# Optimization experiments

Measured on AMD Instinct MI355X. Metric: run time of the kernel, lower is better.

## Reference

```python
import jax, jax.numpy as jnp
import numpy as np

H = 1024       # hidden_size
E = 1024       # embedding_size
V = 50257      # output_size (vocab)
L = 64         # max_length


def setup_inputs() -> dict:
    key = jax.random.key(0)
    ks = jax.random.split(key, 12)
    s = 0.02
    return {
        "input": jax.random.randint(ks[0], (1,), 0, V),
        "hidden": jax.random.normal(ks[1], (1, 1, H), dtype=jnp.float32),
        "encoder_outputs": jax.random.normal(ks[2], (L, H), dtype=jnp.float32),
        "emb": jax.random.normal(ks[3], (V, E), dtype=jnp.float32) * s,
        "attn_w": jax.random.normal(ks[4], (L, H + E), dtype=jnp.float32) * s,
        "attn_b": jnp.zeros((L,), dtype=jnp.float32),
        "comb_w": jax.random.normal(ks[5], (E, H + E), dtype=jnp.float32) * s,
        "comb_b": jnp.zeros((E,), dtype=jnp.float32),
        "w_ih": jax.random.normal(ks[6], (3 * H, E), dtype=jnp.float32) * s,
        "b_ih": jnp.zeros((3 * H,), dtype=jnp.float32),
        "w_hh": jax.random.normal(ks[7], (3 * H, H), dtype=jnp.float32) * s,
        "b_hh": jnp.zeros((3 * H,), dtype=jnp.float32),
        "out_w": jax.random.normal(ks[8], (V, H), dtype=jnp.float32) * s,
        "out_b": jnp.zeros((V,), dtype=jnp.float32),
    }


def reference(input, hidden, encoder_outputs, emb, attn_w, attn_b,
              comb_w, comb_b, w_ih, b_ih, w_hh, b_hh, out_w, out_b):
    # embedding + (dropout = identity in eval)
    embedded = emb[input].reshape(1, E)            # [1, E]
    h0 = hidden[0]                                  # [1, H]
    # Bahdanau-style attention over fixed-length encoder outputs
    attn_logits = jnp.concatenate([embedded, h0], axis=1) @ attn_w.T + attn_b
    attn_weights = jax.nn.softmax(attn_logits, axis=1)      # [1, L]
    attn_applied = attn_weights @ encoder_outputs            # [1, H]
    x = jnp.concatenate([embedded, attn_applied], axis=1) @ comb_w.T + comb_b
    x = jax.nn.relu(x)                               # [1, E]
    # single GRU cell step (torch gate order: r, z, n)
    gi = x @ w_ih.T + b_ih
    gh = h0 @ w_hh.T + b_hh
    i_r, i_z, i_n = jnp.split(gi, 3, axis=1)
    h_r, h_z, h_n = jnp.split(gh, 3, axis=1)
    r = jax.nn.sigmoid(i_r + h_r)
    z = jax.nn.sigmoid(i_z + h_z)
    n = jnp.tanh(i_n + r * h_n)
    h_new = (1.0 - z) * n + z * h0                   # [1, H]
    logp = jax.nn.log_softmax(h_new @ out_w.T + out_b, axis=1)  # [1, V]
    return logp, h_new[None], attn_weights
```

## Files before the change

### kernel.cpp

```cpp
#include <hip/hip_runtime.h>
#include <math.h>

#define H 1024
#define E 1024
#define V 50257
#define L 64
#define HE 2048

__device__ inline float dot4(float4 a, float4 b) {
    return a.x*b.x + a.y*b.y + a.z*b.z + a.w*b.w;
}

__device__ inline float wave_reduce_sum(float v) {
    #pragma unroll
    for (int off = 32; off > 0; off >>= 1)
        v += __shfl_down(v, off, 64);
    return v;
}

__global__ __launch_bounds__(256) void k_lg(
        const int* __restrict__ inp,
        const float* __restrict__ hidden,
        const float* __restrict__ emb,
        const float* __restrict__ attn_w,
        const float* __restrict__ attn_b,
        float* __restrict__ lg) {
    const int b = blockIdx.x;
    const int t = threadIdx.x;
    const int wave = t >> 6, lane = t & 63;
    const float* erow = emb + (size_t)inp[0] * E;
    const float4* e4 = (const float4*)erow;
    const float4* h4 = (const float4*)hidden;
    const float4* w  = (const float4*)(attn_w + (size_t)b * HE);
    float s = dot4(w[t], e4[t]) + dot4(w[256 + t], h4[t]);
    s = wave_reduce_sum(s);
    __shared__ float red[4];
    if (lane == 0) red[wave] = s;
    __syncthreads();
    if (t == 0) lg[b] = red[0] + red[1] + red[2] + red[3] + attn_b[b];
}

__global__ __launch_bounds__(512) void k_comb(
        const int* __restrict__ inp,
        const float* __restrict__ hidden,
        const float* __restrict__ enc,
        const float* __restrict__ emb,
        const float* __restrict__ lg,
        const float* __restrict__ comb_w,
        const float* __restrict__ comb_b,
        float* __restrict__ x,
        float* __restrict__ out_weights) {
    const int bid  = blockIdx.x;
    const int t    = threadIdx.x;
    const int wave = t >> 6;
    const int lane = t & 63;

    __shared__ float sig[L];
    __shared__ __align__(16) float aa[H];

    const float* erow = emb + (size_t)inp[0] * E;
    const float4* e4 = (const float4*)erow;

    if (t < 64) {
        float v = lg[t];
        float m = v;
        #pragma unroll
        for (int off = 32; off > 0; off >>= 1) m = fmaxf(m, __shfl_xor(m, off, 64));
        float ex = expf(v - m);
        float ssum = ex;
        #pragma unroll
        for (int off = 32; off > 0; off >>= 1) ssum += __shfl_xor(ssum, off, 64);
        float w = ex / ssum;
        sig[t] = w;
        if (bid == 0) out_weights[t] = w;
    }
    __syncthreads();
    {
        float a0 = 0.f, a1 = 0.f;
        #pragma unroll 8
        for (int l = 0; l < L; ++l) {
            float sl = sig[l];
            a0 += sl * enc[l * H + t];
            a1 += sl * enc[l * H + t + 512];
        }
        aa[t] = a0;
        aa[t + 512] = a1;
    }
    __syncthreads();
    {
        int row = bid * 8 + wave;
        const float4* wr = (const float4*)(comb_w + (size_t)row * HE);
        const float4* a4 = (const float4*)aa;
        float acc = 0.f;
        #pragma unroll
        for (int i = 0; i < 4; ++i) acc += dot4(wr[i * 64 + lane], e4[i * 64 + lane]);
        #pragma unroll
        for (int i = 0; i < 4; ++i) acc += dot4(wr[256 + i * 64 + lane], a4[i * 64 + lane]);
        acc = wave_reduce_sum(acc);
        if (lane == 0) x[row] = fmaxf(acc + comb_b[row], 0.f);
    }
}

__global__ __launch_bounds__(768) void k_gru(
        const float* __restrict__ x,
        const float* __restrict__ hidden,
        const float* __restrict__ w_ih,
        const float* __restrict__ b_ih,
        const float* __restrict__ w_hh,
        const float* __restrict__ b_hh,
        float* __restrict__ h_new) {
    int t = threadIdx.x, wave = t >> 6, lane = t & 63;
    int g  = wave >> 2;
    int j4 = wave & 3;
    int j  = blockIdx.x * 4 + j4;
    const float4* x4 = (const float4*)x;
    const float4* h4 = (const float4*)hidden;
    const float4* wi = (const float4*)(w_ih + (size_t)(g * H + j) * E);
    const float4* wh = (const float4*)(w_hh + (size_t)(g * H + j) * H);
    float si = 0.f, sh = 0.f;
    #pragma unroll
    for (int i = 0; i < 4; ++i) {
        int idx = i * 64 + lane;
        si += dot4(wi[idx], x4[idx]);
        sh += dot4(wh[idx], h4[idx]);
    }
    #pragma unroll
    for (int off = 32; off > 0; off >>= 1) {
        si += __shfl_down(si, off, 64);
        sh += __shfl_down(sh, off, 64);
    }
    __shared__ float redI[3][4], redH[3][4];
    if (lane == 0) {
        redI[g][j4] = si + b_ih[g * H + j];
        redH[g][j4] = sh + b_hh[g * H + j];
    }
    __syncthreads();
    if (t < 4) {
        int jo = blockIdx.x * 4 + t;
        float i_r = redI[0][t], i_z = redI[1][t], i_n = redI[2][t];
        float h_r = redH[0][t], h_z = redH[1][t], h_n = redH[2][t];
        float r = 1.f / (1.f + expf(-(i_r + h_r)));
        float z = 1.f / (1.f + expf(-(i_z + h_z)));
        float n = tanhf(i_n + r * h_n);
        h_new[jo] = (1.f - z) * n + z * hidden[jo];
    }
}

__global__ __launch_bounds__(256) void k_vocab(
        const float* __restrict__ h_new,
        const float* __restrict__ out_w,
        const float* __restrict__ out_b,
        float* __restrict__ logp,
        float* __restrict__ partials) {
    int t = threadIdx.x, wave = t >> 6, lane = t & 63;
    const float4* h4 = (const float4*)h_new;
    float4 hv[4];
    #pragma unroll
    for (int i = 0; i < 4; ++i) hv[i] = h4[i * 64 + lane];
    int base = blockIdx.x * 16 + wave * 4;
    float s[4] = {0.f, 0.f, 0.f, 0.f};
    if (base + 3 < V) {
        const float4* w0 = (const float4*)(out_w + (size_t)(base + 0) * H);
        const float4* w1 = (const float4*)(out_w + (size_t)(base + 1) * H);
        const float4* w2 = (const float4*)(out_w + (size_t)(base + 2) * H);
        const float4* w3 = (const float4*)(out_w + (size_t)(base + 3) * H);
        #pragma unroll
        for (int i = 0; i < 4; ++i) {
            int idx = i * 64 + lane;
            s[0] += dot4(w0[idx], hv[i]);
            s[1] += dot4(w1[idx], hv[i]);
            s[2] += dot4(w2[idx], hv[i]);
            s[3] += dot4(w3[idx], hv[i]);
        }
    } else {
        #pragma unroll
        for (int k = 0; k < 4; ++k)
            if (base + k < V) {
                const float4* w = (const float4*)(out_w + (size_t)(base + k) * H);
                #pragma unroll
                for (int i = 0; i < 4; ++i) s[k] += dot4(w[i * 64 + lane], hv[i]);
            }
    }
    #pragma unroll
    for (int off = 32; off > 0; off >>= 1) {
        s[0] += __shfl_down(s[0], off, 64);
        s[1] += __shfl_down(s[1], off, 64);
        s[2] += __shfl_down(s[2], off, 64);
        s[3] += __shfl_down(s[3], off, 64);
    }
    __shared__ float smP[4];
    if (lane == 0) {
        float pe = 0.f;
        #pragma unroll
        for (int k = 0; k < 4; ++k) {
            int r = base + k;
            if (r < V) {
                float v = s[k] + out_b[r];
                logp[r] = v;
                pe += expf(v);
            }
        }
        smP[wave] = pe;
    }
    __syncthreads();
    if (t == 0)
        partials[blockIdx.x] = smP[0] + smP[1] + smP[2] + smP[3];
}

__global__ __launch_bounds__(256) void k_lsm(
        float* __restrict__ logp,
        const float* __restrict__ partials, int nb) {
    int t = threadIdx.x;
    float S = 0.f;
    for (int i = t; i < nb; i += 256) S += partials[i];
    S = wave_reduce_sum(S);
    __shared__ float ss[4];
    __shared__ float sh_lz;
    if ((t & 63) == 0) ss[t >> 6] = S;
    __syncthreads();
    if (t == 0) sh_lz = logf(ss[0] + ss[1] + ss[2] + ss[3]);
    __syncthreads();
    float lz = sh_lz;
    int i = blockIdx.x * 256 + t;
    if (i < V) logp[i] -= lz;
}

extern "C" void kernel_launch(void* const* d_in, const int* in_sizes, int n_in,
                              void* d_out, int out_size, void* d_ws, size_t ws_size,
                              hipStream_t stream) {
    const int*   inp     = (const int*)d_in[0];
    const float* hidden  = (const float*)d_in[1];
    const float* enc     = (const float*)d_in[2];
    const float* emb     = (const float*)d_in[3];
    const float* attn_w  = (const float*)d_in[4];
    const float* attn_b  = (const float*)d_in[5];
    const float* comb_w  = (const float*)d_in[6];
    const float* comb_b  = (const float*)d_in[7];
    const float* w_ih    = (const float*)d_in[8];
    const float* b_ih    = (const float*)d_in[9];
    const float* w_hh    = (const float*)d_in[10];
    const float* b_hh    = (const float*)d_in[11];
    const float* out_w   = (const float*)d_in[12];
    const float* out_b   = (const float*)d_in[13];

    float* out          = (float*)d_out;
    float* logp         = out;
    float* h_new        = out + V;
    float* attn_weights = out + V + H;

    float* ws       = (float*)d_ws;
    float* lg       = ws;
    float* x        = ws + 64;
    float* partials = ws + 1088;
    const int nb = (V + 15) / 16;

    k_lg<<<64, 256, 0, stream>>>(inp, hidden, emb, attn_w, attn_b, lg);
    k_comb<<<128, 512, 0, stream>>>(inp, hidden, enc, emb, lg,
                                    comb_w, comb_b, x, attn_weights);
    k_gru<<<256, 768, 0, stream>>>(x, hidden, w_ih, b_ih, w_hh, b_hh, h_new);
    k_vocab<<<nb, 256, 0, stream>>>(h_new, out_w, out_b, logp, partials);
    k_lsm<<<(V + 255) / 256, 256, 0, stream>>>(logp, partials, nb);
}
```

Before: 66.67 us.

## Prefetch output projection weights into cache during early small kernels

Adds extra blocks to the attention-logit, combine and GRU kernels. These blocks stream disjoint thirds of out_w and discard the sums through a never-taken conditional store. The aim is to pull the large vocab weight matrix into the last-level cache while the small, latency-bound kernels underuse memory bandwidth, so the vocab GEMV finds it warm. The cost is extra blocks competing with the real work of those kernels, and the benefit depends on out_w staying resident in cache until k_vocab runs.

```diff
diff --git a/kernel.cpp b/kernel.cpp
--- a/kernel.cpp
+++ b/kernel.cpp
@@ -17,6 +17,25 @@
         v += __shfl_down(v, off, 64);
     return v;
 }
+
+__device__ inline void freight(const float4* __restrict__ src, long lo4, long hi4,
+                               int fb, int nfb, int t, int nt,
+                               float* __restrict__ sink) {
+    long n4 = hi4 - lo4;
+    long per = (n4 + nfb - 1) / nfb;
+    long a = lo4 + (long)fb * per;
+    long b = a + per; if (b > hi4) b = hi4;
+    float acc = 0.f;
+    for (long i = a + t; i < b; i += nt) {
+        float4 v = src[i];
+        acc += v.x + v.y + v.z + v.w;
+    }
+    if (acc == 1.2345e30f) sink[0] = acc;
+}
+
+#define OW_N4   12865792L
+#define OW_A4    4194304L
+#define OW_B4    8388608L
 
 __global__ __launch_bounds__(256) void k_lg(
         const int* __restrict__ inp,
@@ -24,9 +43,15 @@
         const float* __restrict__ emb,
         const float* __restrict__ attn_w,
         const float* __restrict__ attn_b,
-        float* __restrict__ lg) {
+        const float* __restrict__ out_w,
+        float* __restrict__ lg,
+        float* __restrict__ sink) {
     const int b = blockIdx.x;
     const int t = threadIdx.x;
+    if (b >= 64) {
+        freight((const float4*)out_w, 0, OW_A4, b - 64, 960, t, 256, sink);
+        return;
+    }
     const int wave = t >> 6, lane = t & 63;
     const float* erow = emb + (size_t)inp[0] * E;
     const float4* e4 = (const float4*)erow;
@@ -48,10 +73,16 @@
         const float* __restrict__ lg,
         const float* __restrict__ comb_w,
         const float* __restrict__ comb_b,
+        const float* __restrict__ out_w,
         float* __restrict__ x,
-        float* __restrict__ out_weights) {
+        float* __restrict__ out_weights,
+        float* __restrict__ sink) {
     const int bid  = blockIdx.x;
     const int t    = threadIdx.x;
+    if (bid >= 128) {
+        freight((const float4*)out_w, OW_A4, OW_B4, bid - 128, 512, t, 512, sink);
+        return;
+    }
     const int wave = t >> 6;
     const int lane = t & 63;
 
@@ -108,8 +139,14 @@
         const float* __restrict__ b_ih,
         const float* __restrict__ w_hh,
         const float* __restrict__ b_hh,
-        float* __restrict__ h_new) {
+        const float* __restrict__ out_w,
+        float* __restrict__ h_new,
+        float* __restrict__ sink) {
     int t = threadIdx.x, wave = t >> 6, lane = t & 63;
+    if (blockIdx.x >= 256) {
+        freight((const float4*)out_w, OW_B4, OW_N4, blockIdx.x - 256, 512, t, 768, sink);
+        return;
+    }
     int g  = wave >> 2;
     int j4 = wave & 3;
     int j  = blockIdx.x * 4 + j4;
@@ -252,12 +289,13 @@
     float* lg       = ws;
     float* x        = ws + 64;
     float* partials = ws + 1088;
+    float* sink     = ws + 4240;
     const int nb = (V + 15) / 16;
 
-    k_lg<<<64, 256, 0, stream>>>(inp, hidden, emb, attn_w, attn_b, lg);
-    k_comb<<<128, 512, 0, stream>>>(inp, hidden, enc, emb, lg,
-                                    comb_w, comb_b, x, attn_weights);
-    k_gru<<<256, 768, 0, stream>>>(x, hidden, w_ih, b_ih, w_hh, b_hh, h_new);
+    k_lg<<<1024, 256, 0, stream>>>(inp, hidden, emb, attn_w, attn_b, out_w, lg, sink);
+    k_comb<<<640, 512, 0, stream>>>(inp, hidden, enc, emb, lg,
+                                    comb_w, comb_b, out_w, x, attn_weights, sink);
+    k_gru<<<768, 768, 0, stream>>>(x, hidden, w_ih, b_ih, w_hh, b_hh, out_w, h_new, sink);
     k_vocab<<<nb, 256, 0, stream>>>(h_new, out_w, out_b, logp, partials);
     k_lsm<<<(V + 255) / 256, 256, 0, stream>>>(logp, partials, nb);
 }
```

Result: slower. 85.63 us (+28.4%).
